# Kernel tuning notes

Measured on AMD Instinct MI355X. Metric: run time of the kernel, lower is better.

Reference implementation:

```python
import jax, jax.numpy as jnp
import numpy as np

NUM_EDGE_TYPES = 8
HIDDEN = 128
N_NODES = 50000
N_EDGES = 600000


def setup_inputs() -> dict:
    key = jax.random.key(0)
    ks = jax.random.split(key, 10)
    H = HIDDEN
    h = jax.random.normal(ks[0], (N_NODES, H), dtype=jnp.float32)
    edge_index = jax.random.randint(ks[1], (2, N_EDGES), 0, N_NODES, dtype=jnp.int32)
    edge_type = jax.random.randint(ks[2], (N_EDGES,), 0, NUM_EDGE_TYPES + 1, dtype=jnp.int32)
    s = 1.0 / np.sqrt(H)
    W_msg = jax.random.uniform(ks[3], (H, H), jnp.float32, -s, s)
    b_msg = jax.random.uniform(ks[4], (H,), jnp.float32, -s, s)
    edge_embed = jax.random.normal(ks[5], (NUM_EDGE_TYPES + 1, H), dtype=jnp.float32)
    W_ih = jax.random.uniform(ks[6], (3 * H, H), jnp.float32, -s, s)
    W_hh = jax.random.uniform(ks[7], (3 * H, H), jnp.float32, -s, s)
    b_ih = jax.random.uniform(ks[8], (3 * H,), jnp.float32, -s, s)
    b_hh = jax.random.uniform(ks[9], (3 * H,), jnp.float32, -s, s)
    return {"h": h, "edge_index": edge_index, "edge_type": edge_type,
            "num_nodes": N_NODES, "W_msg": W_msg, "b_msg": b_msg,
            "edge_embed": edge_embed, "W_ih": W_ih, "W_hh": W_hh,
            "b_ih": b_ih, "b_hh": b_hh}


def _gru_cell(x, h, W_ih, W_hh, b_ih, b_hh):
    # PyTorch GRUCell: gates ordered (r, z, n)
    H = h.shape[-1]
    gi = x @ W_ih.T + b_ih  # (N, 3H)
    gh = h @ W_hh.T + b_hh
    i_r, i_z, i_n = gi[:, :H], gi[:, H:2 * H], gi[:, 2 * H:]
    h_r, h_z, h_n = gh[:, :H], gh[:, H:2 * H], gh[:, 2 * H:]
    r = jax.nn.sigmoid(i_r + h_r)
    z = jax.nn.sigmoid(i_z + h_z)
    n = jnp.tanh(i_n + r * h_n)
    return (1.0 - z) * n + z * h


def reference(h, edge_index, edge_type, num_nodes, W_msg, b_msg, edge_embed, W_ih, W_hh, b_ih, b_hh):
    src = edge_index[0]
    dst = edge_index[1]
    # gather -> linear -> edge-type embed add
    src_h = h[src] @ W_msg.T + b_msg                      # (E, H)
    emb = edge_embed[jnp.clip(edge_type, 0, NUM_EDGE_TYPES)]  # (E, H)
    msg = src_h + emb
    # scatter-add into per-node message buffer
    messages = jax.ops.segment_sum(msg, dst, num_segments=num_nodes)  # (num_nodes, H)
    h_new = _gru_cell(messages, h[:num_nodes], W_ih, W_hh, b_ih, b_hh)
    result = jnp.zeros_like(h).at[:num_nodes].set(h_new)
    return result
```

## Files before the change

### kernel.cpp

```cpp
#include <hip/hip_runtime.h>
#include <math.h>

#define H 128
typedef unsigned int u32;
typedef unsigned long long u64;
typedef __attribute__((ext_vector_type(8))) short short8;
typedef __attribute__((ext_vector_type(4))) float floatx4;

#define XS_STRIDE 136
#define CS_STRIDE 40

#define SCAN_B 64
#define SCAN_T 256

__device__ __forceinline__ float sigmoid_f(float x) {
    return 1.0f / (1.0f + __expf(-x));
}
__device__ __forceinline__ float tanh_f(float x) {
    float t = __expf(-2.0f * fabsf(x));
    float r = (1.0f - t) / (1.0f + t);
    return copysignf(r, x);
}
__device__ __forceinline__ unsigned short f2bf(float x) {
    u32 u = __float_as_uint(x);
    return (unsigned short)((u + 0x7fffu + ((u >> 16) & 1u)) >> 16);
}
__device__ __forceinline__ float bf2f(unsigned short s) {
    return __uint_as_float(((u32)s) << 16);
}
__device__ __forceinline__ float bf_lo32(u32 u) { return __uint_as_float(u << 16); }
__device__ __forceinline__ float bf_hi32(u32 u) { return __uint_as_float(u & 0xffff0000u); }

__global__ __launch_bounds__(256) void fused_pre_kernel(
    const float* __restrict__ h, unsigned short* __restrict__ h_b, int total8,
    int* __restrict__ deg, int N,
    const float* __restrict__ Wih, const float* __restrict__ Whh,
    const float* __restrict__ Wm,  const float* __restrict__ emb,
    const float* __restrict__ bm,
    unsigned short* __restrict__ Wcs, unsigned short* __restrict__ Whhs,
    unsigned short* __restrict__ embWs, int HB, int DB)
{
    int b = blockIdx.x;
    if (b < HB) {
        int idx = b * 256 + threadIdx.x;
        if (idx >= total8) return;
        const float4* p = (const float4*)(h + (size_t)idx * 8);
        float4 a = p[0], bb = p[1];
        short8 v;
        v[0] = (short)f2bf(a.x);  v[1] = (short)f2bf(a.y);
        v[2] = (short)f2bf(a.z);  v[3] = (short)f2bf(a.w);
        v[4] = (short)f2bf(bb.x); v[5] = (short)f2bf(bb.y);
        v[6] = (short)f2bf(bb.z); v[7] = (short)f2bf(bb.w);
        *(short8*)(h_b + (size_t)idx * 8) = v;
        return;
    }
    if (b < HB + DB) {
        int idx = (b - HB) * 256 + threadIdx.x;
        if (idx < N) deg[idx] = 0;
        return;
    }
    int idx = (b - HB - DB) * 256 + threadIdx.x;
    if (idx < 49152) {
        int g = idx >> 7;
        int k = idx & 127;
        float acc = 0.f;
#pragma unroll 4
        for (int c = 0; c < H; ++c)
            acc += Wih[(size_t)g * H + c] * Wm[(size_t)c * H + k];
        int gate = g >> 7;
        int wi = g & 127;
        int j = wi >> 4, m = wi & 15;
        int kc = k >> 5, q = (k >> 3) & 3, i = k & 7;
        int l = q * 16 + m;
        Wcs[(size_t)(((gate * 8 + j) * 4 + kc) * 64 + l) * 8 + i] = f2bf(acc);
    } else if (idx < 61440) {
        int s = idx - 49152;
        int i = s & 7;
        int l = (s >> 3) & 63;
        int jb = s >> 9;
        int gate = jb >> 3, jj = jb & 7;
        int q = l >> 4, m = l & 15;
        int t = q * 8 + i;
        unsigned short v = 0;
        if (t < 9) {
            int g = gate * 128 + jj * 16 + m;
            float acc = 0.f;
#pragma unroll 4
            for (int jx = 0; jx < H; ++jx)
                acc += (emb[(size_t)t * H + jx] + bm[jx]) * Wih[(size_t)g * H + jx];
            v = f2bf(acc);
        }
        embWs[s] = v;
    } else if (idx < 67584) {
        int t2 = idx - 61440;
        int l  = t2 & 63;
        int kc = (t2 >> 6) & 3;
        int jr = t2 >> 8;
        int m = l & 15, q = l >> 4;
        size_t srco = (size_t)(jr * 16 + m) * H + kc * 32 + q * 8;
        const float4* s0 = (const float4*)(Whh + srco);
        float4 a = s0[0], bb = s0[1];
        short8 v;
        v[0] = (short)f2bf(a.x);  v[1] = (short)f2bf(a.y);
        v[2] = (short)f2bf(a.z);  v[3] = (short)f2bf(a.w);
        v[4] = (short)f2bf(bb.x); v[5] = (short)f2bf(bb.y);
        v[6] = (short)f2bf(bb.z); v[7] = (short)f2bf(bb.w);
        *(short8*)(Whhs + (size_t)t2 * 8) = v;
    }
}

__global__ __launch_bounds__(256) void hist_kernel(
    const int* __restrict__ eidx, int* __restrict__ deg, int E)
{
    int e = blockIdx.x * 256 + threadIdx.x;
    if (e < E) atomicAdd(&deg[eidx[E + e]], 1);
}

__global__ __launch_bounds__(SCAN_T) void scan_part_kernel(
    const int* __restrict__ deg, int* __restrict__ tsum,
    int* __restrict__ bsum, int N, int ipt)
{
    __shared__ int red[SCAN_T];
    int t = threadIdx.x;
    int g = blockIdx.x * SCAN_T + t;
    int s = g * ipt;
    int e = s + ipt < N ? s + ipt : N;
    int sum = 0;
    for (int i = s; i < e; ++i) sum += deg[i];
    tsum[g] = sum;
    red[t] = sum;
    __syncthreads();
    for (int d = SCAN_T / 2; d > 0; d >>= 1) {
        if (t < d) red[t] += red[t + d];
        __syncthreads();
    }
    if (t == 0) bsum[blockIdx.x] = red[0];
}

__global__ __launch_bounds__(SCAN_T) void scan_final_kernel(
    const int* __restrict__ deg, const int* __restrict__ tsum,
    const int* __restrict__ bsum, int* __restrict__ off,
    int* __restrict__ pos, int N, int ipt)
{
    __shared__ int part[SCAN_T];
    __shared__ int bpre[SCAN_B + 1];
    int t = threadIdx.x;
    if (t == 0) {
        int acc = 0;
        for (int b2 = 0; b2 < SCAN_B; ++b2) { bpre[b2] = acc; acc += bsum[b2]; }
        bpre[SCAN_B] = acc;
        if (blockIdx.x == 0) off[N] = acc;
    }
    int g = blockIdx.x * SCAN_T + t;
    part[t] = tsum[g];
    __syncthreads();
    for (int d = 1; d < SCAN_T; d <<= 1) {
        int v = (t >= d) ? part[t - d] : 0;
        __syncthreads();
        part[t] += v;
        __syncthreads();
    }
    int base = bpre[blockIdx.x] + ((t == 0) ? 0 : part[t - 1]);
    int s = g * ipt;
    int e = s + ipt < N ? s + ipt : N;
    for (int i = s; i < e; ++i) {
        off[i] = base;
        pos[i] = base;
        base += deg[i];
    }
}

__global__ __launch_bounds__(256) void fill_kernel(
    const int* __restrict__ eidx, const int* __restrict__ etype,
    int* __restrict__ pos, int* __restrict__ packed, int E)
{
    int e = blockIdx.x * 256 + threadIdx.x;
    if (e >= E) return;
    int src = eidx[e];
    int dst = eidx[E + e];
    int t = etype[e];
    t = t < 0 ? 0 : (t > 8 ? 8 : t);
    int p = atomicAdd(&pos[dst], 1);
    packed[p] = src | (t << 24);
}

__global__ __launch_bounds__(256) void gather_kernel(
    const unsigned short* __restrict__ h_b,
    const int* __restrict__ off, const int* __restrict__ packed,
    unsigned short* __restrict__ S_b, u64* __restrict__ cnt, int N)
{
    int n = blockIdx.x * 4 + (threadIdx.x >> 6);
    if (n >= N) return;
    int lane = threadIdx.x & 63;
    int b = off[n], e = off[n + 1];
    float ax = 0.f, ay = 0.f;
    u64 c = 0;
    int i = b;
    for (; i + 4 <= e; i += 4) {
        int u0 = packed[i + 0];
        int u1 = packed[i + 1];
        int u2 = packed[i + 2];
        int u3 = packed[i + 3];
        u32 x0 = *((const u32*)(h_b + (size_t)(u0 & 0xffffff) * H) + lane);
        u32 x1 = *((const u32*)(h_b + (size_t)(u1 & 0xffffff) * H) + lane);
        u32 x2 = *((const u32*)(h_b + (size_t)(u2 & 0xffffff) * H) + lane);
        u32 x3 = *((const u32*)(h_b + (size_t)(u3 & 0xffffff) * H) + lane);
        c += (1ull << (7 * (u0 >> 24))) + (1ull << (7 * (u1 >> 24)))
           + (1ull << (7 * (u2 >> 24))) + (1ull << (7 * (u3 >> 24)));
        ax += bf_lo32(x0) + bf_lo32(x1) + bf_lo32(x2) + bf_lo32(x3);
        ay += bf_hi32(x0) + bf_hi32(x1) + bf_hi32(x2) + bf_hi32(x3);
    }
    for (; i < e; ++i) {
        int u = packed[i];
        u32 x = *((const u32*)(h_b + (size_t)(u & 0xffffff) * H) + lane);
        c += 1ull << (7 * (u >> 24));
        ax += bf_lo32(x);
        ay += bf_hi32(x);
    }
    u32 o = (u32)f2bf(ax) | ((u32)f2bf(ay) << 16);
    *((u32*)(S_b + (size_t)n * H) + lane) = o;
    if (lane == 0) cnt[n] = c;
}

__global__ __launch_bounds__(256, 2) void gru_mfma_kernel(
    const unsigned short* __restrict__ S_b, const unsigned short* __restrict__ h_b,
    const unsigned short* __restrict__ Wcs, const unsigned short* __restrict__ Whhs,
    const unsigned short* __restrict__ embWs,
    const float* __restrict__ bih, const float* __restrict__ bhh,
    const u64* __restrict__ cnt,
    const int* __restrict__ numn, float* __restrict__ out, int N)
{
    __shared__ unsigned short xs[64 * XS_STRIDE];
    __shared__ unsigned short hsb[64 * XS_STRIDE];
    __shared__ unsigned short cs[64 * CS_STRIDE];

    int tid = threadIdx.x;
    int node0 = blockIdx.x * 64;

    for (int c = tid; c < 1024; c += 256) {
        int r = c >> 4;
        int k8 = (c & 15) << 3;
        int n = node0 + r;
        int nc = n < N ? n : N - 1;
        *(short8*)(&xs[r * XS_STRIDE + k8]) =
            *(const short8*)(S_b + (size_t)nc * H + k8);
        *(short8*)(&hsb[r * XS_STRIDE + k8]) =
            *(const short8*)(h_b + (size_t)nc * H + k8);
    }
    {
        int r = tid >> 2, tg = tid & 3;
        int n = node0 + r;
        u64 cv = cnt[n < N ? n : N - 1];
        short8 v = {0, 0, 0, 0, 0, 0, 0, 0};
        if (tg == 0) {
#pragma unroll
            for (int i = 0; i < 8; ++i)
                v[i] = (short)f2bf((float)((u32)(cv >> (7 * i)) & 127u));
        } else if (tg == 1) {
            v[0] = (short)f2bf((float)((u32)(cv >> 56) & 127u));
        }
        *(short8*)(&cs[r * CS_STRIDE + tg * 8]) = v;
    }
    __syncthreads();

    int lane = tid & 63;
    int wv = tid >> 6;
    int am = lane & 15;
    int aq = lane >> 4;

    int num_nodes = numn[0];
    floatx4 zero = {0.f, 0.f, 0.f, 0.f};

#pragma unroll
    for (int jj = 0; jj < 2; ++jj) {
        int j = wv * 2 + jj;
        floatx4 aR[4], aZ[4], aIn[4], aHn[4];
        {
            short8 er = *(const short8*)(embWs + (size_t)((0 * 8 + j) * 64 + lane) * 8);
            short8 ez = *(const short8*)(embWs + (size_t)((1 * 8 + j) * 64 + lane) * 8);
            short8 en = *(const short8*)(embWs + (size_t)((2 * 8 + j) * 64 + lane) * 8);
#pragma unroll
            for (int rt = 0; rt < 4; ++rt) {
                short8 acn = *(const short8*)(&cs[(rt * 16 + am) * CS_STRIDE + aq * 8]);
                aR[rt]  = __builtin_amdgcn_mfma_f32_16x16x32_bf16(acn, er, zero, 0, 0, 0);
                aZ[rt]  = __builtin_amdgcn_mfma_f32_16x16x32_bf16(acn, ez, zero, 0, 0, 0);
                aIn[rt] = __builtin_amdgcn_mfma_f32_16x16x32_bf16(acn, en, zero, 0, 0, 0);
                aHn[rt] = zero;
            }
        }
#pragma unroll
        for (int kc = 0; kc < 4; ++kc) {
            size_t c_r = (size_t)(((0 * 8 + j) * 4 + kc) * 64 + lane) * 8;
            size_t c_z = (size_t)(((1 * 8 + j) * 4 + kc) * 64 + lane) * 8;
            size_t c_n = (size_t)(((2 * 8 + j) * 4 + kc) * 64 + lane) * 8;
            short8 bir = *(const short8*)(Wcs + c_r);
            short8 bhr = *(const short8*)(Whhs + c_r);
            short8 biz = *(const short8*)(Wcs + c_z);
            short8 bhz = *(const short8*)(Whhs + c_z);
            short8 bin = *(const short8*)(Wcs + c_n);
            short8 bhn = *(const short8*)(Whhs + c_n);
#pragma unroll
            for (int rt = 0; rt < 4; ++rt) {
                int arow = rt * 16 + am;
                short8 axv = *(const short8*)(&xs[arow * XS_STRIDE + kc * 32 + aq * 8]);
                short8 ahv = *(const short8*)(&hsb[arow * XS_STRIDE + kc * 32 + aq * 8]);
                aR[rt]  = __builtin_amdgcn_mfma_f32_16x16x32_bf16(axv, bir, aR[rt], 0, 0, 0);
                aR[rt]  = __builtin_amdgcn_mfma_f32_16x16x32_bf16(ahv, bhr, aR[rt], 0, 0, 0);
                aZ[rt]  = __builtin_amdgcn_mfma_f32_16x16x32_bf16(axv, biz, aZ[rt], 0, 0, 0);
                aZ[rt]  = __builtin_amdgcn_mfma_f32_16x16x32_bf16(ahv, bhz, aZ[rt], 0, 0, 0);
                aIn[rt] = __builtin_amdgcn_mfma_f32_16x16x32_bf16(axv, bin, aIn[rt], 0, 0, 0);
                aHn[rt] = __builtin_amdgcn_mfma_f32_16x16x32_bf16(ahv, bhn, aHn[rt], 0, 0, 0);
            }
        }
        int c = j * 16 + am;
        float b_r = bih[c]       + bhh[c];
        float b_z = bih[128 + c] + bhh[128 + c];
        float b_in = bih[256 + c], b_hn = bhh[256 + c];
#pragma unroll
        for (int rt = 0; rt < 4; ++rt) {
#pragma unroll
            for (int q = 0; q < 4; ++q) {
                int m = rt * 16 + aq * 4 + q;
                int node = node0 + m;
                if (node < N) {
                    float r  = sigmoid_f(aR[rt][q] + b_r);
                    float z  = sigmoid_f(aZ[rt][q] + b_z);
                    float nv = tanh_f((aIn[rt][q] + b_in) + r * (aHn[rt][q] + b_hn));
                    float hv = bf2f(hsb[m * XS_STRIDE + c]);
                    float o  = (1.0f - z) * nv + z * hv;
                    out[(size_t)node * H + c] = (node < num_nodes) ? o : 0.0f;
                }
            }
        }
    }
}

extern "C" void kernel_launch(void* const* d_in, const int* in_sizes, int n_in,
                              void* d_out, int out_size, void* d_ws, size_t ws_size,
                              hipStream_t stream) {
    const float* h    = (const float*)d_in[0];
    const int*  eidx  = (const int*)d_in[1];
    const int*  etype = (const int*)d_in[2];
    const int*  numn  = (const int*)d_in[3];
    const float* Wm   = (const float*)d_in[4];
    const float* bm   = (const float*)d_in[5];
    const float* emb  = (const float*)d_in[6];
    const float* Wih  = (const float*)d_in[7];
    const float* Whh  = (const float*)d_in[8];
    const float* bih  = (const float*)d_in[9];
    const float* bhh  = (const float*)d_in[10];

    int N = in_sizes[0] / H;
    int E = in_sizes[2];

    unsigned short* S_b   = (unsigned short*)d_ws;
    unsigned short* h_b   = S_b + (size_t)N * H;
    unsigned short* Wcs   = h_b + (size_t)N * H;
    unsigned short* Whhs  = Wcs + 3 * H * H;
    unsigned short* embWs = Whhs + 3 * H * H;
    u64* cnt    = (u64*)(embWs + 12288);
    int* deg    = (int*)(cnt + N);
    int* pos    = deg + N;
    int* off    = pos + N;
    int* packed = off + (N + 1);
    int* tsum   = packed + E;
    int* bsum   = tsum + SCAN_B * SCAN_T;

    int total8 = N * H / 8;
    int HB = (total8 + 255) / 256;
    int DB = (N + 255) / 256;
    int PB = 264;
    fused_pre_kernel<<<HB + DB + PB, 256, 0, stream>>>(
        h, h_b, total8, deg, N, Wih, Whh, Wm, emb, bm, Wcs, Whhs, embWs, HB, DB);

    hist_kernel<<<(E + 255) / 256, 256, 0, stream>>>(eidx, deg, E);

    int ipt = (N + SCAN_B * SCAN_T - 1) / (SCAN_B * SCAN_T);
    scan_part_kernel<<<SCAN_B, SCAN_T, 0, stream>>>(deg, tsum, bsum, N, ipt);
    scan_final_kernel<<<SCAN_B, SCAN_T, 0, stream>>>(deg, tsum, bsum, off, pos, N, ipt);

    fill_kernel<<<(E + 255) / 256, 256, 0, stream>>>(eidx, etype, pos, packed, E);

    gather_kernel<<<(N + 3) / 4, 256, 0, stream>>>(h_b, off, packed, S_b, cnt, N);

    int nblk64 = (N + 63) / 64;
    gru_mfma_kernel<<<nblk64, 256, 0, stream>>>(S_b, h_b, Wcs, Whhs, embWs,
                                                bih, bhh, cnt, numn, (float*)d_out, N);
}
```

Before: 233.5 us.

## Split GRU kernel across column halves and unroll gather by eight

The GRU MFMA kernel now launches two blocks per 64-node tile, each computing half of the output columns with one column group per wave, and raises the occupancy hint to four blocks per CU. The gather kernel adds an 8-wide unrolled loop so more independent row loads are in flight per wave. The aim is more parallelism and latency hiding in both kernels. In exchange, each node tile's x, h and count data are loaded into shared memory twice.

New measurement: 225.9 us. 1.03x faster.

```diff
diff --git a/kernel.cpp b/kernel.cpp
--- a/kernel.cpp
+++ b/kernel.cpp
@@ -196,6 +196,32 @@
     float ax = 0.f, ay = 0.f;
     u64 c = 0;
     int i = b;
+    for (; i + 8 <= e; i += 8) {
+        int u0 = packed[i + 0];
+        int u1 = packed[i + 1];
+        int u2 = packed[i + 2];
+        int u3 = packed[i + 3];
+        int u4 = packed[i + 4];
+        int u5 = packed[i + 5];
+        int u6 = packed[i + 6];
+        int u7 = packed[i + 7];
+        u32 x0 = *((const u32*)(h_b + (size_t)(u0 & 0xffffff) * H) + lane);
+        u32 x1 = *((const u32*)(h_b + (size_t)(u1 & 0xffffff) * H) + lane);
+        u32 x2 = *((const u32*)(h_b + (size_t)(u2 & 0xffffff) * H) + lane);
+        u32 x3 = *((const u32*)(h_b + (size_t)(u3 & 0xffffff) * H) + lane);
+        u32 x4 = *((const u32*)(h_b + (size_t)(u4 & 0xffffff) * H) + lane);
+        u32 x5 = *((const u32*)(h_b + (size_t)(u5 & 0xffffff) * H) + lane);
+        u32 x6 = *((const u32*)(h_b + (size_t)(u6 & 0xffffff) * H) + lane);
+        u32 x7 = *((const u32*)(h_b + (size_t)(u7 & 0xffffff) * H) + lane);
+        c += (1ull << (7 * (u0 >> 24))) + (1ull << (7 * (u1 >> 24)))
+           + (1ull << (7 * (u2 >> 24))) + (1ull << (7 * (u3 >> 24)))
+           + (1ull << (7 * (u4 >> 24))) + (1ull << (7 * (u5 >> 24)))
+           + (1ull << (7 * (u6 >> 24))) + (1ull << (7 * (u7 >> 24)));
+        ax += bf_lo32(x0) + bf_lo32(x1) + bf_lo32(x2) + bf_lo32(x3)
+            + bf_lo32(x4) + bf_lo32(x5) + bf_lo32(x6) + bf_lo32(x7);
+        ay += bf_hi32(x0) + bf_hi32(x1) + bf_hi32(x2) + bf_hi32(x3)
+            + bf_hi32(x4) + bf_hi32(x5) + bf_hi32(x6) + bf_hi32(x7);
+    }
     for (; i + 4 <= e; i += 4) {
         int u0 = packed[i + 0];
         int u1 = packed[i + 1];
@@ -222,7 +248,7 @@
     if (lane == 0) cnt[n] = c;
 }
 
-__global__ __launch_bounds__(256, 2) void gru_mfma_kernel(
+__global__ __launch_bounds__(256, 4) void gru_mfma_kernel(
     const unsigned short* __restrict__ S_b, const unsigned short* __restrict__ h_b,
     const unsigned short* __restrict__ Wcs, const unsigned short* __restrict__ Whhs,
     const unsigned short* __restrict__ embWs,
@@ -235,7 +261,17 @@
     __shared__ unsigned short cs[64 * CS_STRIDE];
 
     int tid = threadIdx.x;
-    int node0 = blockIdx.x * 64;
+    int bx = blockIdx.x;
+    int node0 = (bx >> 1) * 64;
+    int jhalf = bx & 1;
+
+    int lane = tid & 63;
+    int wv = tid >> 6;
+    int j = jhalf * 4 + wv;
+
+    short8 er = *(const short8*)(embWs + (size_t)((0 * 8 + j) * 64 + lane) * 8);
+    short8 ez = *(const short8*)(embWs + (size_t)((1 * 8 + j) * 64 + lane) * 8);
+    short8 en = *(const short8*)(embWs + (size_t)((2 * 8 + j) * 64 + lane) * 8);
 
     for (int c = tid; c < 1024; c += 256) {
         int r = c >> 4;
@@ -263,73 +299,62 @@
     }
     __syncthreads();
 
-    int lane = tid & 63;
-    int wv = tid >> 6;
     int am = lane & 15;
     int aq = lane >> 4;
 
     int num_nodes = numn[0];
     floatx4 zero = {0.f, 0.f, 0.f, 0.f};
 
-#pragma unroll
-    for (int jj = 0; jj < 2; ++jj) {
-        int j = wv * 2 + jj;
-        floatx4 aR[4], aZ[4], aIn[4], aHn[4];
-        {
-            short8 er = *(const short8*)(embWs + (size_t)((0 * 8 + j) * 64 + lane) * 8);
-            short8 ez = *(const short8*)(embWs + (size_t)((1 * 8 + j) * 64 + lane) * 8);
-            short8 en = *(const short8*)(embWs + (size_t)((2 * 8 + j) * 64 + lane) * 8);
-#pragma unroll
-            for (int rt = 0; rt < 4; ++rt) {
-                short8 acn = *(const short8*)(&cs[(rt * 16 + am) * CS_STRIDE + aq * 8]);
-                aR[rt]  = __builtin_amdgcn_mfma_f32_16x16x32_bf16(acn, er, zero, 0, 0, 0);
-                aZ[rt]  = __builtin_amdgcn_mfma_f32_16x16x32_bf16(acn, ez, zero, 0, 0, 0);
-                aIn[rt] = __builtin_amdgcn_mfma_f32_16x16x32_bf16(acn, en, zero, 0, 0, 0);
-                aHn[rt] = zero;
-            }
+    floatx4 aR[4], aZ[4], aIn[4], aHn[4];
+#pragma unroll
+    for (int rt = 0; rt < 4; ++rt) {
+        short8 acn = *(const short8*)(&cs[(rt * 16 + am) * CS_STRIDE + aq * 8]);
+        aR[rt]  = __builtin_amdgcn_mfma_f32_16x16x32_bf16(acn, er, zero, 0, 0, 0);
+        aZ[rt]  = __builtin_amdgcn_mfma_f32_16x16x32_bf16(acn, ez, zero, 0, 0, 0);
+        aIn[rt] = __builtin_amdgcn_mfma_f32_16x16x32_bf16(acn, en, zero, 0, 0, 0);
+        aHn[rt] = zero;
+    }
+#pragma unroll
+    for (int kc = 0; kc < 4; ++kc) {
+        size_t c_r = (size_t)(((0 * 8 + j) * 4 + kc) * 64 + lane) * 8;
+        size_t c_z = (size_t)(((1 * 8 + j) * 4 + kc) * 64 + lane) * 8;
+        size_t c_n = (size_t)(((2 * 8 + j) * 4 + kc) * 64 + lane) * 8;
+        short8 bir = *(const short8*)(Wcs + c_r);
+        short8 bhr = *(const short8*)(Whhs + c_r);
+        short8 biz = *(const short8*)(Wcs + c_z);
+        short8 bhz = *(const short8*)(Whhs + c_z);
+        short8 bin = *(const short8*)(Wcs + c_n);
+        short8 bhn = *(const short8*)(Whhs + c_n);
+#pragma unroll
+        for (int rt = 0; rt < 4; ++rt) {
+            int arow = rt * 16 + am;
+            short8 axv = *(const short8*)(&xs[arow * XS_STRIDE + kc * 32 + aq * 8]);
+            short8 ahv = *(const short8*)(&hsb[arow * XS_STRIDE + kc * 32 + aq * 8]);
+            aR[rt]  = __builtin_amdgcn_mfma_f32_16x16x32_bf16(axv, bir, aR[rt], 0, 0, 0);
+            aR[rt]  = __builtin_amdgcn_mfma_f32_16x16x32_bf16(ahv, bhr, aR[rt], 0, 0, 0);
+            aZ[rt]  = __builtin_amdgcn_mfma_f32_16x16x32_bf16(axv, biz, aZ[rt], 0, 0, 0);
+            aZ[rt]  = __builtin_amdgcn_mfma_f32_16x16x32_bf16(ahv, bhz, aZ[rt], 0, 0, 0);
+            aIn[rt] = __builtin_amdgcn_mfma_f32_16x16x32_bf16(axv, bin, aIn[rt], 0, 0, 0);
+            aHn[rt] = __builtin_amdgcn_mfma_f32_16x16x32_bf16(ahv, bhn, aHn[rt], 0, 0, 0);
         }
-#pragma unroll
-        for (int kc = 0; kc < 4; ++kc) {
-            size_t c_r = (size_t)(((0 * 8 + j) * 4 + kc) * 64 + lane) * 8;
-            size_t c_z = (size_t)(((1 * 8 + j) * 4 + kc) * 64 + lane) * 8;
-            size_t c_n = (size_t)(((2 * 8 + j) * 4 + kc) * 64 + lane) * 8;
-            short8 bir = *(const short8*)(Wcs + c_r);
-            short8 bhr = *(const short8*)(Whhs + c_r);
-            short8 biz = *(const short8*)(Wcs + c_z);
-            short8 bhz = *(const short8*)(Whhs + c_z);
-            short8 bin = *(const short8*)(Wcs + c_n);
-            short8 bhn = *(const short8*)(Whhs + c_n);
-#pragma unroll
-            for (int rt = 0; rt < 4; ++rt) {
-                int arow = rt * 16 + am;
-                short8 axv = *(const short8*)(&xs[arow * XS_STRIDE + kc * 32 + aq * 8]);
-                short8 ahv = *(const short8*)(&hsb[arow * XS_STRIDE + kc * 32 + aq * 8]);
-                aR[rt]  = __builtin_amdgcn_mfma_f32_16x16x32_bf16(axv, bir, aR[rt], 0, 0, 0);
-                aR[rt]  = __builtin_amdgcn_mfma_f32_16x16x32_bf16(ahv, bhr, aR[rt], 0, 0, 0);
-                aZ[rt]  = __builtin_amdgcn_mfma_f32_16x16x32_bf16(axv, biz, aZ[rt], 0, 0, 0);
-                aZ[rt]  = __builtin_amdgcn_mfma_f32_16x16x32_bf16(ahv, bhz, aZ[rt], 0, 0, 0);
-                aIn[rt] = __builtin_amdgcn_mfma_f32_16x16x32_bf16(axv, bin, aIn[rt], 0, 0, 0);
-                aHn[rt] = __builtin_amdgcn_mfma_f32_16x16x32_bf16(ahv, bhn, aHn[rt], 0, 0, 0);
-            }
-        }
-        int c = j * 16 + am;
-        float b_r = bih[c]       + bhh[c];
-        float b_z = bih[128 + c] + bhh[128 + c];
-        float b_in = bih[256 + c], b_hn = bhh[256 + c];
-#pragma unroll
-        for (int rt = 0; rt < 4; ++rt) {
-#pragma unroll
-            for (int q = 0; q < 4; ++q) {
-                int m = rt * 16 + aq * 4 + q;
-                int node = node0 + m;
-                if (node < N) {
-                    float r  = sigmoid_f(aR[rt][q] + b_r);
-                    float z  = sigmoid_f(aZ[rt][q] + b_z);
-                    float nv = tanh_f((aIn[rt][q] + b_in) + r * (aHn[rt][q] + b_hn));
-                    float hv = bf2f(hsb[m * XS_STRIDE + c]);
-                    float o  = (1.0f - z) * nv + z * hv;
-                    out[(size_t)node * H + c] = (node < num_nodes) ? o : 0.0f;
-                }
+    }
+    int c = j * 16 + am;
+    float b_r = bih[c]       + bhh[c];
+    float b_z = bih[128 + c] + bhh[128 + c];
+    float b_in = bih[256 + c], b_hn = bhh[256 + c];
+#pragma unroll
+    for (int rt = 0; rt < 4; ++rt) {
+#pragma unroll
+        for (int q = 0; q < 4; ++q) {
+            int m = rt * 16 + aq * 4 + q;
+            int node = node0 + m;
+            if (node < N) {
+                float r  = sigmoid_f(aR[rt][q] + b_r);
+                float z  = sigmoid_f(aZ[rt][q] + b_z);
+                float nv = tanh_f((aIn[rt][q] + b_in) + r * (aHn[rt][q] + b_hn));
+                float hv = bf2f(hsb[m * XS_STRIDE + c]);
+                float o  = (1.0f - z) * nv + z * hv;
+                out[(size_t)node * H + c] = (node < num_nodes) ? o : 0.0f;
             }
         }
     }
@@ -383,7 +408,7 @@
 
     gather_kernel<<<(N + 3) / 4, 256, 0, stream>>>(h_b, off, packed, S_b, cnt, N);
 
-    int nblk64 = (N + 63) / 64;
-    gru_mfma_kernel<<<nblk64, 256, 0, stream>>>(S_b, h_b, Wcs, Whhs, embWs,
-                                                bih, bhh, cnt, numn, (float*)d_out, N);
-}
+    int nblk = ((N + 63) / 64) * 2;
+    gru_mfma_kernel<<<nblk, 256, 0, stream>>>(S_b, h_b, Wcs, Whhs, embWs,
+                                              bih, bhh, cnt, numn, (float*)d_out, N);
+}
```

## Replace CSR build with atomic linked lists and split GRU output columns across blocks

Applied to the files above, without the earlier changes.

Swaps the histogram, two-pass scan and CSR fill for per-destination linked lists built with atomicExch, which removes three kernel launches and their serial dependency. The gather walks four nodes' lists at once per wave so their pointer-chasing latencies overlap. The GRU kernel is split so each block computes half of the output columns, doubling the block count and raising the occupancy bound to 4, at the cost of loading and staging the same node tile in two blocks. Linked-list traversal makes dependent, scattered loads and gives a nondeterministic summation order.

New measurement: 222.3 us. -4.8%, faster.

```diff
diff --git a/kernel.cpp b/kernel.cpp
--- a/kernel.cpp
+++ b/kernel.cpp
@@ -10,9 +10,6 @@
 #define XS_STRIDE 136
 #define CS_STRIDE 40
 
-#define SCAN_B 64
-#define SCAN_T 256
-
 __device__ __forceinline__ float sigmoid_f(float x) {
     return 1.0f / (1.0f + __expf(-x));
 }
@@ -33,7 +30,7 @@
 
 __global__ __launch_bounds__(256) void fused_pre_kernel(
     const float* __restrict__ h, unsigned short* __restrict__ h_b, int total8,
-    int* __restrict__ deg, int N,
+    int* __restrict__ head, int N,
     const float* __restrict__ Wih, const float* __restrict__ Whh,
     const float* __restrict__ Wm,  const float* __restrict__ emb,
     const float* __restrict__ bm,
@@ -56,7 +53,7 @@
     }
     if (b < HB + DB) {
         int idx = (b - HB) * 256 + threadIdx.x;
-        if (idx < N) deg[idx] = 0;
+        if (idx < N) head[idx] = -1;
         return;
     }
     int idx = (b - HB - DB) * 256 + threadIdx.x;
@@ -109,70 +106,10 @@
     }
 }
 
-__global__ __launch_bounds__(256) void hist_kernel(
-    const int* __restrict__ eidx, int* __restrict__ deg, int E)
-{
-    int e = blockIdx.x * 256 + threadIdx.x;
-    if (e < E) atomicAdd(&deg[eidx[E + e]], 1);
-}
-
-__global__ __launch_bounds__(SCAN_T) void scan_part_kernel(
-    const int* __restrict__ deg, int* __restrict__ tsum,
-    int* __restrict__ bsum, int N, int ipt)
-{
-    __shared__ int red[SCAN_T];
-    int t = threadIdx.x;
-    int g = blockIdx.x * SCAN_T + t;
-    int s = g * ipt;
-    int e = s + ipt < N ? s + ipt : N;
-    int sum = 0;
-    for (int i = s; i < e; ++i) sum += deg[i];
-    tsum[g] = sum;
-    red[t] = sum;
-    __syncthreads();
-    for (int d = SCAN_T / 2; d > 0; d >>= 1) {
-        if (t < d) red[t] += red[t + d];
-        __syncthreads();
-    }
-    if (t == 0) bsum[blockIdx.x] = red[0];
-}
-
-__global__ __launch_bounds__(SCAN_T) void scan_final_kernel(
-    const int* __restrict__ deg, const int* __restrict__ tsum,
-    const int* __restrict__ bsum, int* __restrict__ off,
-    int* __restrict__ pos, int N, int ipt)
-{
-    __shared__ int part[SCAN_T];
-    __shared__ int bpre[SCAN_B + 1];
-    int t = threadIdx.x;
-    if (t == 0) {
-        int acc = 0;
-        for (int b2 = 0; b2 < SCAN_B; ++b2) { bpre[b2] = acc; acc += bsum[b2]; }
-        bpre[SCAN_B] = acc;
-        if (blockIdx.x == 0) off[N] = acc;
-    }
-    int g = blockIdx.x * SCAN_T + t;
-    part[t] = tsum[g];
-    __syncthreads();
-    for (int d = 1; d < SCAN_T; d <<= 1) {
-        int v = (t >= d) ? part[t - d] : 0;
-        __syncthreads();
-        part[t] += v;
-        __syncthreads();
-    }
-    int base = bpre[blockIdx.x] + ((t == 0) ? 0 : part[t - 1]);
-    int s = g * ipt;
-    int e = s + ipt < N ? s + ipt : N;
-    for (int i = s; i < e; ++i) {
-        off[i] = base;
-        pos[i] = base;
-        base += deg[i];
-    }
-}
-
-__global__ __launch_bounds__(256) void fill_kernel(
+__global__ __launch_bounds__(256) void fill_ll_kernel(
     const int* __restrict__ eidx, const int* __restrict__ etype,
-    int* __restrict__ pos, int* __restrict__ packed, int E)
+    int* __restrict__ head, int* __restrict__ nexte,
+    int* __restrict__ packed, int E)
 {
     int e = blockIdx.x * 256 + threadIdx.x;
     if (e >= E) return;
@@ -180,49 +117,84 @@
     int dst = eidx[E + e];
     int t = etype[e];
     t = t < 0 ? 0 : (t > 8 ? 8 : t);
-    int p = atomicAdd(&pos[dst], 1);
-    packed[p] = src | (t << 24);
-}
-
-__global__ __launch_bounds__(256) void gather_kernel(
+    packed[e] = src | (t << 24);
+    int old = atomicExch(&head[dst], e);
+    nexte[e] = old;
+}
+
+__global__ __launch_bounds__(256) void gather_ll_kernel(
     const unsigned short* __restrict__ h_b,
-    const int* __restrict__ off, const int* __restrict__ packed,
+    const int* __restrict__ head, const int* __restrict__ nexte,
+    const int* __restrict__ packed,
     unsigned short* __restrict__ S_b, u64* __restrict__ cnt, int N)
 {
-    int n = blockIdx.x * 4 + (threadIdx.x >> 6);
-    if (n >= N) return;
+    int w = blockIdx.x * 4 + (threadIdx.x >> 6);
     int lane = threadIdx.x & 63;
-    int b = off[n], e = off[n + 1];
-    float ax = 0.f, ay = 0.f;
-    u64 c = 0;
-    int i = b;
-    for (; i + 4 <= e; i += 4) {
-        int u0 = packed[i + 0];
-        int u1 = packed[i + 1];
-        int u2 = packed[i + 2];
-        int u3 = packed[i + 3];
-        u32 x0 = *((const u32*)(h_b + (size_t)(u0 & 0xffffff) * H) + lane);
-        u32 x1 = *((const u32*)(h_b + (size_t)(u1 & 0xffffff) * H) + lane);
-        u32 x2 = *((const u32*)(h_b + (size_t)(u2 & 0xffffff) * H) + lane);
-        u32 x3 = *((const u32*)(h_b + (size_t)(u3 & 0xffffff) * H) + lane);
-        c += (1ull << (7 * (u0 >> 24))) + (1ull << (7 * (u1 >> 24)))
-           + (1ull << (7 * (u2 >> 24))) + (1ull << (7 * (u3 >> 24)));
-        ax += bf_lo32(x0) + bf_lo32(x1) + bf_lo32(x2) + bf_lo32(x3);
-        ay += bf_hi32(x0) + bf_hi32(x1) + bf_hi32(x2) + bf_hi32(x3);
-    }
-    for (; i < e; ++i) {
-        int u = packed[i];
-        u32 x = *((const u32*)(h_b + (size_t)(u & 0xffffff) * H) + lane);
-        c += 1ull << (7 * (u >> 24));
-        ax += bf_lo32(x);
-        ay += bf_hi32(x);
-    }
-    u32 o = (u32)f2bf(ax) | ((u32)f2bf(ay) << 16);
-    *((u32*)(S_b + (size_t)n * H) + lane) = o;
-    if (lane == 0) cnt[n] = c;
-}
-
-__global__ __launch_bounds__(256, 2) void gru_mfma_kernel(
+    int n0 = w * 4;
+    if (n0 >= N) return;
+
+    int e0 = head[n0];
+    int e1 = (n0 + 1 < N) ? head[n0 + 1] : -1;
+    int e2 = (n0 + 2 < N) ? head[n0 + 2] : -1;
+    int e3 = (n0 + 3 < N) ? head[n0 + 3] : -1;
+
+    float ax0 = 0.f, ay0 = 0.f, ax1 = 0.f, ay1 = 0.f;
+    float ax2 = 0.f, ay2 = 0.f, ax3 = 0.f, ay3 = 0.f;
+    u64 c0 = 0, c1 = 0, c2 = 0, c3 = 0;
+
+    while ((e0 >= 0) || (e1 >= 0) || (e2 >= 0) || (e3 >= 0)) {
+        int nx0 = -1, nx1 = -1, nx2 = -1, nx3 = -1;
+        int u0 = 0, u1 = 0, u2 = 0, u3 = 0;
+        if (e0 >= 0) { nx0 = nexte[e0]; u0 = packed[e0]; }
+        if (e1 >= 0) { nx1 = nexte[e1]; u1 = packed[e1]; }
+        if (e2 >= 0) { nx2 = nexte[e2]; u2 = packed[e2]; }
+        if (e3 >= 0) { nx3 = nexte[e3]; u3 = packed[e3]; }
+        if (e0 >= 0) {
+            u32 x = *((const u32*)(h_b + (size_t)(u0 & 0xffffff) * H) + lane);
+            c0 += 1ull << (7 * (u0 >> 24));
+            ax0 += bf_lo32(x); ay0 += bf_hi32(x);
+        }
+        if (e1 >= 0) {
+            u32 x = *((const u32*)(h_b + (size_t)(u1 & 0xffffff) * H) + lane);
+            c1 += 1ull << (7 * (u1 >> 24));
+            ax1 += bf_lo32(x); ay1 += bf_hi32(x);
+        }
+        if (e2 >= 0) {
+            u32 x = *((const u32*)(h_b + (size_t)(u2 & 0xffffff) * H) + lane);
+            c2 += 1ull << (7 * (u2 >> 24));
+            ax2 += bf_lo32(x); ay2 += bf_hi32(x);
+        }
+        if (e3 >= 0) {
+            u32 x = *((const u32*)(h_b + (size_t)(u3 & 0xffffff) * H) + lane);
+            c3 += 1ull << (7 * (u3 >> 24));
+            ax3 += bf_lo32(x); ay3 += bf_hi32(x);
+        }
+        e0 = nx0; e1 = nx1; e2 = nx2; e3 = nx3;
+    }
+
+    {
+        u32 o = (u32)f2bf(ax0) | ((u32)f2bf(ay0) << 16);
+        *((u32*)(S_b + (size_t)n0 * H) + lane) = o;
+        if (lane == 0) cnt[n0] = c0;
+    }
+    if (n0 + 1 < N) {
+        u32 o = (u32)f2bf(ax1) | ((u32)f2bf(ay1) << 16);
+        *((u32*)(S_b + (size_t)(n0 + 1) * H) + lane) = o;
+        if (lane == 0) cnt[n0 + 1] = c1;
+    }
+    if (n0 + 2 < N) {
+        u32 o = (u32)f2bf(ax2) | ((u32)f2bf(ay2) << 16);
+        *((u32*)(S_b + (size_t)(n0 + 2) * H) + lane) = o;
+        if (lane == 0) cnt[n0 + 2] = c2;
+    }
+    if (n0 + 3 < N) {
+        u32 o = (u32)f2bf(ax3) | ((u32)f2bf(ay3) << 16);
+        *((u32*)(S_b + (size_t)(n0 + 3) * H) + lane) = o;
+        if (lane == 0) cnt[n0 + 3] = c3;
+    }
+}
+
+__global__ __launch_bounds__(256, 4) void gru_mfma_kernel(
     const unsigned short* __restrict__ S_b, const unsigned short* __restrict__ h_b,
     const unsigned short* __restrict__ Wcs, const unsigned short* __restrict__ Whhs,
     const unsigned short* __restrict__ embWs,
@@ -235,7 +207,17 @@
     __shared__ unsigned short cs[64 * CS_STRIDE];
 
     int tid = threadIdx.x;
-    int node0 = blockIdx.x * 64;
+    int bx = blockIdx.x;
+    int node0 = (bx >> 1) * 64;
+    int jhalf = bx & 1;
+
+    int lane = tid & 63;
+    int wv = tid >> 6;
+    int j = jhalf * 4 + wv;
+
+    short8 er = *(const short8*)(embWs + (size_t)((0 * 8 + j) * 64 + lane) * 8);
+    short8 ez = *(const short8*)(embWs + (size_t)((1 * 8 + j) * 64 + lane) * 8);
+    short8 en = *(const short8*)(embWs + (size_t)((2 * 8 + j) * 64 + lane) * 8);
 
     for (int c = tid; c < 1024; c += 256) {
         int r = c >> 4;
@@ -263,73 +245,62 @@
     }
     __syncthreads();
 
-    int lane = tid & 63;
-    int wv = tid >> 6;
     int am = lane & 15;
     int aq = lane >> 4;
 
     int num_nodes = numn[0];
     floatx4 zero = {0.f, 0.f, 0.f, 0.f};
 
-#pragma unroll
-    for (int jj = 0; jj < 2; ++jj) {
-        int j = wv * 2 + jj;
-        floatx4 aR[4], aZ[4], aIn[4], aHn[4];
-        {
-            short8 er = *(const short8*)(embWs + (size_t)((0 * 8 + j) * 64 + lane) * 8);
-            short8 ez = *(const short8*)(embWs + (size_t)((1 * 8 + j) * 64 + lane) * 8);
-            short8 en = *(const short8*)(embWs + (size_t)((2 * 8 + j) * 64 + lane) * 8);
-#pragma unroll
-            for (int rt = 0; rt < 4; ++rt) {
-                short8 acn = *(const short8*)(&cs[(rt * 16 + am) * CS_STRIDE + aq * 8]);
-                aR[rt]  = __builtin_amdgcn_mfma_f32_16x16x32_bf16(acn, er, zero, 0, 0, 0);
-                aZ[rt]  = __builtin_amdgcn_mfma_f32_16x16x32_bf16(acn, ez, zero, 0, 0, 0);
-                aIn[rt] = __builtin_amdgcn_mfma_f32_16x16x32_bf16(acn, en, zero, 0, 0, 0);
-                aHn[rt] = zero;
-            }
-        }
-#pragma unroll
-        for (int kc = 0; kc < 4; ++kc) {
-            size_t c_r = (size_t)(((0 * 8 + j) * 4 + kc) * 64 + lane) * 8;
-            size_t c_z = (size_t)(((1 * 8 + j) * 4 + kc) * 64 + lane) * 8;
-            size_t c_n = (size_t)(((2 * 8 + j) * 4 + kc) * 64 + lane) * 8;
-            short8 bir = *(const short8*)(Wcs + c_r);
-            short8 bhr = *(const short8*)(Whhs + c_r);
-            short8 biz = *(const short8*)(Wcs + c_z);
-            short8 bhz = *(const short8*)(Whhs + c_z);
-            short8 bin = *(const short8*)(Wcs + c_n);
-            short8 bhn = *(const short8*)(Whhs + c_n);
-#pragma unroll
-            for (int rt = 0; rt < 4; ++rt) {
-                int arow = rt * 16 + am;
-                short8 axv = *(const short8*)(&xs[arow * XS_STRIDE + kc * 32 + aq * 8]);
-                short8 ahv = *(const short8*)(&hsb[arow * XS_STRIDE + kc * 32 + aq * 8]);
-                aR[rt]  = __builtin_amdgcn_mfma_f32_16x16x32_bf16(axv, bir, aR[rt], 0, 0, 0);
-                aR[rt]  = __builtin_amdgcn_mfma_f32_16x16x32_bf16(ahv, bhr, aR[rt], 0, 0, 0);
-                aZ[rt]  = __builtin_amdgcn_mfma_f32_16x16x32_bf16(axv, biz, aZ[rt], 0, 0, 0);
-                aZ[rt]  = __builtin_amdgcn_mfma_f32_16x16x32_bf16(ahv, bhz, aZ[rt], 0, 0, 0);
-                aIn[rt] = __builtin_amdgcn_mfma_f32_16x16x32_bf16(axv, bin, aIn[rt], 0, 0, 0);
-                aHn[rt] = __builtin_amdgcn_mfma_f32_16x16x32_bf16(ahv, bhn, aHn[rt], 0, 0, 0);
-            }
-        }
-        int c = j * 16 + am;
-        float b_r = bih[c]       + bhh[c];
-        float b_z = bih[128 + c] + bhh[128 + c];
-        float b_in = bih[256 + c], b_hn = bhh[256 + c];
+    floatx4 aR[4], aZ[4], aIn[4], aHn[4];
+#pragma unroll
+    for (int rt = 0; rt < 4; ++rt) {
+        short8 acn = *(const short8*)(&cs[(rt * 16 + am) * CS_STRIDE + aq * 8]);
+        aR[rt]  = __builtin_amdgcn_mfma_f32_16x16x32_bf16(acn, er, zero, 0, 0, 0);
+        aZ[rt]  = __builtin_amdgcn_mfma_f32_16x16x32_bf16(acn, ez, zero, 0, 0, 0);
+        aIn[rt] = __builtin_amdgcn_mfma_f32_16x16x32_bf16(acn, en, zero, 0, 0, 0);
+        aHn[rt] = zero;
+    }
+#pragma unroll
+    for (int kc = 0; kc < 4; ++kc) {
+        size_t c_r = (size_t)(((0 * 8 + j) * 4 + kc) * 64 + lane) * 8;
+        size_t c_z = (size_t)(((1 * 8 + j) * 4 + kc) * 64 + lane) * 8;
+        size_t c_n = (size_t)(((2 * 8 + j) * 4 + kc) * 64 + lane) * 8;
+        short8 bir = *(const short8*)(Wcs + c_r);
+        short8 bhr = *(const short8*)(Whhs + c_r);
+        short8 biz = *(const short8*)(Wcs + c_z);
+        short8 bhz = *(const short8*)(Whhs + c_z);
+        short8 bin = *(const short8*)(Wcs + c_n);
+        short8 bhn = *(const short8*)(Whhs + c_n);
 #pragma unroll
         for (int rt = 0; rt < 4; ++rt) {
-#pragma unroll
-            for (int q = 0; q < 4; ++q) {
-                int m = rt * 16 + aq * 4 + q;
-                int node = node0 + m;
-                if (node < N) {
-                    float r  = sigmoid_f(aR[rt][q] + b_r);
-                    float z  = sigmoid_f(aZ[rt][q] + b_z);
-                    float nv = tanh_f((aIn[rt][q] + b_in) + r * (aHn[rt][q] + b_hn));
-                    float hv = bf2f(hsb[m * XS_STRIDE + c]);
-                    float o  = (1.0f - z) * nv + z * hv;
-                    out[(size_t)node * H + c] = (node < num_nodes) ? o : 0.0f;
-                }
+            int arow = rt * 16 + am;
+            short8 axv = *(const short8*)(&xs[arow * XS_STRIDE + kc * 32 + aq * 8]);
+            short8 ahv = *(const short8*)(&hsb[arow * XS_STRIDE + kc * 32 + aq * 8]);
+            aR[rt]  = __builtin_amdgcn_mfma_f32_16x16x32_bf16(axv, bir, aR[rt], 0, 0, 0);
+            aR[rt]  = __builtin_amdgcn_mfma_f32_16x16x32_bf16(ahv, bhr, aR[rt], 0, 0, 0);
+            aZ[rt]  = __builtin_amdgcn_mfma_f32_16x16x32_bf16(axv, biz, aZ[rt], 0, 0, 0);
+            aZ[rt]  = __builtin_amdgcn_mfma_f32_16x16x32_bf16(ahv, bhz, aZ[rt], 0, 0, 0);
+            aIn[rt] = __builtin_amdgcn_mfma_f32_16x16x32_bf16(axv, bin, aIn[rt], 0, 0, 0);
+            aHn[rt] = __builtin_amdgcn_mfma_f32_16x16x32_bf16(ahv, bhn, aHn[rt], 0, 0, 0);
+        }
+    }
+    int c = j * 16 + am;
+    float b_r = bih[c]       + bhh[c];
+    float b_z = bih[128 + c] + bhh[128 + c];
+    float b_in = bih[256 + c], b_hn = bhh[256 + c];
+#pragma unroll
+    for (int rt = 0; rt < 4; ++rt) {
+#pragma unroll
+        for (int q = 0; q < 4; ++q) {
+            int m = rt * 16 + aq * 4 + q;
+            int node = node0 + m;
+            if (node < N) {
+                float r  = sigmoid_f(aR[rt][q] + b_r);
+                float z  = sigmoid_f(aZ[rt][q] + b_z);
+                float nv = tanh_f((aIn[rt][q] + b_in) + r * (aHn[rt][q] + b_hn));
+                float hv = bf2f(hsb[m * XS_STRIDE + c]);
+                float o  = (1.0f - z) * nv + z * hv;
+                out[(size_t)node * H + c] = (node < num_nodes) ? o : 0.0f;
             }
         }
     }
@@ -359,31 +330,24 @@
     unsigned short* Whhs  = Wcs + 3 * H * H;
     unsigned short* embWs = Whhs + 3 * H * H;
     u64* cnt    = (u64*)(embWs + 12288);
-    int* deg    = (int*)(cnt + N);
-    int* pos    = deg + N;
-    int* off    = pos + N;
-    int* packed = off + (N + 1);
-    int* tsum   = packed + E;
-    int* bsum   = tsum + SCAN_B * SCAN_T;
+    int* head   = (int*)(cnt + N);
+    int* packed = head + N;
+    int* nexte  = packed + E;
 
     int total8 = N * H / 8;
     int HB = (total8 + 255) / 256;
     int DB = (N + 255) / 256;
     int PB = 264;
     fused_pre_kernel<<<HB + DB + PB, 256, 0, stream>>>(
-        h, h_b, total8, deg, N, Wih, Whh, Wm, emb, bm, Wcs, Whhs, embWs, HB, DB);
-
-    hist_kernel<<<(E + 255) / 256, 256, 0, stream>>>(eidx, deg, E);
-
-    int ipt = (N + SCAN_B * SCAN_T - 1) / (SCAN_B * SCAN_T);
-    scan_part_kernel<<<SCAN_B, SCAN_T, 0, stream>>>(deg, tsum, bsum, N, ipt);
-    scan_final_kernel<<<SCAN_B, SCAN_T, 0, stream>>>(deg, tsum, bsum, off, pos, N, ipt);
-
-    fill_kernel<<<(E + 255) / 256, 256, 0, stream>>>(eidx, etype, pos, packed, E);
-
-    gather_kernel<<<(N + 3) / 4, 256, 0, stream>>>(h_b, off, packed, S_b, cnt, N);
-
-    int nblk64 = (N + 63) / 64;
-    gru_mfma_kernel<<<nblk64, 256, 0, stream>>>(S_b, h_b, Wcs, Whhs, embWs,
-                                                bih, bhh, cnt, numn, (float*)d_out, N);
-}
+        h, h_b, total8, head, N, Wih, Whh, Wm, emb, bm, Wcs, Whhs, embWs, HB, DB);
+
+    fill_ll_kernel<<<(E + 255) / 256, 256, 0, stream>>>(
+        eidx, etype, head, nexte, packed, E);
+
+    gather_ll_kernel<<<(N + 15) / 16, 256, 0, stream>>>(
+        h_b, head, nexte, packed, S_b, cnt, N);
+
+    int nblk = ((N + 63) / 64) * 2;
+    gru_mfma_kernel<<<nblk, 256, 0, stream>>>(S_b, h_b, Wcs, Whhs, embWs,
+                                              bih, bhh, cnt, numn, (float*)d_out, N);
+}
```
